# Kernel optimization log

Measured on AMD Instinct MI355X. Metric: run time of the kernel, lower is better.

The kernel has to match this reference:

```python
import jax, jax.numpy as jnp
import numpy as np
from jax import lax

SQRT_HALF = np.float32(np.sqrt(0.5))


def glu_block(x, pad_mask, w, b):
    # x: [B,T,D], pad_mask: [B,T] True=padded, w: [2D,D,3], b: [2D]
    x = jnp.where(pad_mask[..., None], 0.0, x)
    xc = jnp.transpose(x, (0, 2, 1))  # [B,D,T]
    y = lax.conv_general_dilated(xc, w, (1,), 'SAME',
                                 dimension_numbers=('NCH', 'OIH', 'NCH'))
    y = y + b[None, :, None]
    y = jnp.transpose(y, (0, 2, 1))  # [B,T,2D]
    a, g = jnp.split(y, 2, axis=-1)
    out = a * jax.nn.sigmoid(g)
    return (out + x) * SQRT_HALF


def setup_inputs() -> dict:
    key = jax.random.key(0)
    ks = jax.random.split(key, 12)
    B, T_MEL, T_PH, D, V, MEL_D = 32, 2000, 512, 256, 100, 80
    mels = jax.random.normal(ks[0], (B, T_MEL, MEL_D), dtype=jnp.float32)
    phonemes = jax.random.randint(ks[1], (B, T_PH), 0, V)
    mel_lens = jax.random.randint(ks[2], (B,), 1, T_MEL)
    phoneme_lens = jax.random.randint(ks[3], (B,), 1, T_PH)
    embedding = 0.02 * jax.random.normal(ks[4], (V, D), dtype=jnp.float32)
    mel_conv_w = 0.02 * jax.random.normal(ks[5], (D, MEL_D, 3), dtype=jnp.float32)
    mel_conv_b = jnp.zeros((D,), dtype=jnp.float32)
    ph_w = 0.02 * jax.random.normal(ks[6], (4, 2 * D, D, 3), dtype=jnp.float32)
    ph_b = jnp.zeros((4, 2 * D), dtype=jnp.float32)
    mel_w = 0.02 * jax.random.normal(ks[7], (4, 2 * D, D, 3), dtype=jnp.float32)
    mel_b = jnp.zeros((4, 2 * D), dtype=jnp.float32)
    return {"mels": mels, "phonemes": phonemes, "mel_lens": mel_lens,
            "phoneme_lens": phoneme_lens, "embedding": embedding,
            "mel_conv_w": mel_conv_w, "mel_conv_b": mel_conv_b,
            "ph_w": ph_w, "ph_b": ph_b, "mel_w": mel_w, "mel_b": mel_b}


def reference(mels, phonemes, mel_lens, phoneme_lens, embedding,
              mel_conv_w, mel_conv_b, ph_w, ph_b, mel_w, mel_b):
    B, T_mel, _ = mels.shape
    # --- mel encoder ---
    mel_mask = jnp.arange(T_mel)[None, :] >= mel_lens[:, None]  # [B,T_mel]
    mc = lax.conv_general_dilated(jnp.transpose(mels, (0, 2, 1)), mel_conv_w,
                                  (1,), 'SAME',
                                  dimension_numbers=('NCH', 'OIH', 'NCH'))
    mel_enc = jnp.transpose(mc + mel_conv_b[None, :, None], (0, 2, 1))
    for i in range(4):
        mel_enc = glu_block(mel_enc, mel_mask, mel_w[i], mel_b[i])
    # --- phoneme encoder (prepend blank index 0) ---
    ph = jnp.pad(phonemes, ((0, 0), (1, 0)), constant_values=0)  # [B,T_ph+1]
    T_ph1 = ph.shape[1]
    ph_mask = jnp.arange(T_ph1)[None, :] > phoneme_lens[:, None]  # [B,T_ph+1]
    ph_enc = embedding[ph]  # [B,T_ph+1,D]
    for i in range(4):
        ph_enc = glu_block(ph_enc, ph_mask, ph_w[i], ph_b[i])
    # --- negative squared pairwise L2 distances, masked over padded phonemes ---
    mel_sq = jnp.sum(mel_enc * mel_enc, axis=-1)  # [B,T_mel]
    ph_sq = jnp.sum(ph_enc * ph_enc, axis=-1)     # [B,T_ph+1]
    dots = jnp.einsum('btd,bsd->bts', mel_enc, ph_enc)  # [B,T_mel,T_ph+1]
    distances = 2.0 * dots - mel_sq[:, :, None] - ph_sq[:, None, :]
    distances = jnp.where(ph_mask[:, None, :], -1e9, distances)
    attn = jax.nn.softmax(distances, axis=2)
    context = jnp.einsum('bts,bsd->btd', attn, ph_enc)
    return jnp.concatenate([mel_enc, context], axis=2)  # [B,T_mel,2D]
```

## Files before the change

### kernel.cpp

```cpp
#include <hip/hip_runtime.h>

typedef _Float16 f16;
typedef __attribute__((ext_vector_type(8))) _Float16 half8;
typedef __attribute__((ext_vector_type(4))) _Float16 half4;
typedef __attribute__((ext_vector_type(4))) float f32x4;

__device__ inline f32x4 mfma16(half8 a, half8 b, f32x4 c) {
  return __builtin_amdgcn_mfma_f32_16x16x32_f16(a, b, c, 0, 0, 0);
}

__global__ void prep_wtglu_kernel(const float* __restrict__ mel_w,
                                  const float* __restrict__ ph_w,
                                  f16* __restrict__ wt) {
  int bid = blockIdx.x;
  int p = bid % 12, lby = bid / 12;
  int by = lby & 3, l = lby >> 2;
  int cb = p / 3, tap = p - cb * 3;
  const float* src = (l < 4) ? (mel_w + (size_t)l * 512 * 256 * 3)
                             : (ph_w + (size_t)(l - 4) * 512 * 256 * 3);
  f16* dst = wt + (size_t)bid * 8192;
  int tid = threadIdx.x;
#pragma unroll
  for (int k = 0; k < 4; ++k) {
    int s = tid + k * 256;
    int lane = s & 63, rest = s >> 6;
    int kc = rest & 1, nt = (rest >> 1) & 3, wc = rest >> 3;
    int rg = by * 128 + wc * 64 + nt * 16 + (lane & 15);
    int n32 = rg >> 5, j = rg & 31;
    int ch = (j < 16) ? (n32 * 16 + j) : (256 + n32 * 16 + (j - 16));
    int i0 = cb * 64 + kc * 32 + (lane >> 4) * 8;
#pragma unroll
    for (int e = 0; e < 8; ++e)
      dst[(size_t)s * 8 + e] = (f16)src[((size_t)ch * 256 + i0 + e) * 3 + tap];
  }
}

__global__ void prep_wt0_kernel(const float* __restrict__ w, f16* __restrict__ wt0) {
  int idx = blockIdx.x * 256 + threadIdx.x;
  const int total = 256 * 288;
  if (idx >= total) return;
  int o = idx / 288, k = idx % 288;
  int tap = k / 96, i = k % 96;
  wt0[idx] = (i < 80) ? (f16)w[((size_t)o * 80 + i) * 3 + tap] : (f16)0.f;
}

__global__ void embed_kernel(const int* __restrict__ phon, const float* __restrict__ emb,
                             f16* __restrict__ out) {
  int s = blockIdx.x, b = blockIdx.y;
  int lane = threadIdx.x;
  int tok = (s == 0) ? 0 : phon[b * 512 + (s - 1)];
  float4 f = *(const float4*)(emb + (size_t)tok * 256 + lane * 4);
  half4 h = {(f16)f.x, (f16)f.y, (f16)f.z, (f16)f.w};
  *(half4*)(out + ((size_t)b * 513 + s) * 256 + lane * 4) = h;
}

__global__ __launch_bounds__(256) void conv0_kernel(
    const float* __restrict__ mels, const f16* __restrict__ wt0,
    const float* __restrict__ bias, f16* __restrict__ out) {
  __shared__ f16 xs[66 * 104];
  __shared__ f16 ws[64 * 104];
  const int tid = threadIdx.x;
  const int b = blockIdx.z;
  const int t0 = blockIdx.x * 64;
  const int by = blockIdx.y;

  for (int idx = tid; idx < 66 * 24; idx += 256) {
    int r = idx / 24, v = idx % 24;
    int t = t0 - 1 + r;
    half4 h = {0.f, 0.f, 0.f, 0.f};
    if (t >= 0 && t < 2000 && v < 20) {
      float4 f = *(const float4*)(mels + ((size_t)b * 2000 + t) * 80 + v * 4);
      h[0] = (f16)f.x; h[1] = (f16)f.y; h[2] = (f16)f.z; h[3] = (f16)f.w;
    }
    *(half4*)(xs + r * 104 + v * 4) = h;
  }
  const int lane = tid & 63, wv = tid >> 6;
  const int wr = wv >> 1, wc = wv & 1;
  const int l15 = lane & 15, q = lane >> 4;
  f32x4 acc[2][2] = {};
  const f16* wrow = wt0 + (size_t)(by * 64) * 288;
  for (int tap = 0; tap < 3; ++tap) {
    __syncthreads();
    for (int idx = tid; idx < 64 * 12; idx += 256) {
      int r = idx / 12, v = idx % 12;
      *(half8*)(ws + r * 104 + v * 8) =
          *(const half8*)(wrow + (size_t)r * 288 + tap * 96 + v * 8);
    }
    __syncthreads();
#pragma unroll
    for (int s2 = 0; s2 < 3; ++s2) {
      int ch = s2 * 32 + q * 8;
      half8 a0 = *(const half8*)(xs + (32 * wr + l15 + tap) * 104 + ch);
      half8 a1 = *(const half8*)(xs + (32 * wr + 16 + l15 + tap) * 104 + ch);
      half8 b0 = *(const half8*)(ws + (32 * wc + l15) * 104 + ch);
      half8 b1 = *(const half8*)(ws + (32 * wc + 16 + l15) * 104 + ch);
      acc[0][0] = mfma16(a0, b0, acc[0][0]);
      acc[0][1] = mfma16(a0, b1, acc[0][1]);
      acc[1][0] = mfma16(a1, b0, acc[1][0]);
      acc[1][1] = mfma16(a1, b1, acc[1][1]);
    }
  }
#pragma unroll
  for (int rf = 0; rf < 2; ++rf)
#pragma unroll
    for (int cf = 0; cf < 2; ++cf) {
      int c = by * 64 + 32 * wc + 16 * cf + l15;
      float bb = bias[c];
#pragma unroll
      for (int r = 0; r < 4; ++r) {
        int t = t0 + 32 * wr + 16 * rf + 4 * q + r;
        if (t < 2000)
          out[((size_t)b * 2000 + t) * 256 + c] = (f16)(acc[rf][cf][r] + bb);
      }
    }
}

__device__ __forceinline__ void glu_body(
    f16* xs,
    const f16* __restrict__ x, const f16* __restrict__ wt,
    const float* __restrict__ bias, f16* __restrict__ out,
    const int* __restrict__ lens, int lenAdd, int T, int TT, int writeConst,
    int bx, int by, int b) {
  const int tid = threadIdx.x;
  const int tt = (bx + b) % TT;
  const int t0 = tt * 128;
  int thr = lens[b] + lenAdd;
  if (thr > T) thr = T;
  const size_t xbase = (size_t)b * T * 256;
  const int lane = tid & 63, wv = tid >> 6;
  const int wr = wv >> 1, wc = wv & 1;
  const int l15 = lane & 15, q = lane >> 4;

  if (t0 > thr) {
    if (writeConst) {
#pragma unroll
      for (int p = 0; p < 2; ++p) {
        int n32 = by * 4 + wc * 2 + p;
        int c = n32 * 16 + l15;
        float ba = bias[c], bg = bias[256 + c];
        f16 o = (f16)((ba * (1.0f / (1.0f + __expf(-bg)))) * 0.70710678118f);
#pragma unroll
        for (int mt = 0; mt < 4; ++mt)
#pragma unroll
          for (int rr = 0; rr < 4; ++rr) {
            int t = t0 + wr * 64 + mt * 16 + q * 4 + rr;
            if (t < T) out[xbase + (size_t)t * 256 + c] = o;
          }
      }
    }
    return;
  }

  f32x4 acc[4][4] = {};
  const f16* wby = wt + (size_t)by * 12 * 8192 + (size_t)wc * 4096 + (size_t)lane * 8;

  half8 xr[5];
  half8 wb[4][2], wn[4][2];
  auto loadX = [&](int cb) {
#pragma unroll
    for (int it = 0; it < 5; ++it) {
      int idx = tid + it * 256;
      half8 val = {};
      if (idx < 1040) {
        int lr = idx >> 3, v = idx & 7;
        int trow = t0 - 1 + lr;
        if (trow >= 0 && trow < thr)
          val = *(const half8*)(x + xbase + (size_t)trow * 256 + cb * 64 + v * 8);
      }
      xr[it] = val;
    }
  };
  auto storeX = [&]() {
#pragma unroll
    for (int it = 0; it < 5; ++it) {
      int idx = tid + it * 256;
      if (idx < 1040) {
        int lr = idx >> 3, v = idx & 7;
        *(half8*)(xs + lr * 72 + v * 8) = xr[it];
      }
    }
  };
  auto loadWreg = [&](half8 W[4][2], int p) {
    const f16* wp = wby + (size_t)p * 8192;
#pragma unroll
    for (int nt = 0; nt < 4; ++nt)
#pragma unroll
      for (int kc = 0; kc < 2; ++kc)
        W[nt][kc] = *(const half8*)(wp + (nt * 2 + kc) * 512);
  };

  loadX(0);
  loadWreg(wb, 0);

#pragma unroll
  for (int cb = 0; cb < 4; ++cb) {
    __syncthreads();
    storeX();
    __syncthreads();
    if (cb < 3) loadX(cb + 1);
#pragma unroll
    for (int tap = 0; tap < 3; ++tap) {
      const int p = cb * 3 + tap;
      if (p < 11) loadWreg(wn, p + 1);

      half8 af[4][2];
#pragma unroll
      for (int mt = 0; mt < 4; ++mt)
#pragma unroll
        for (int kc = 0; kc < 2; ++kc)
          af[mt][kc] = *(const half8*)(xs + (wr * 64 + mt * 16 + l15 + tap) * 72 + kc * 32 + q * 8);
      __builtin_amdgcn_s_setprio(1);
#pragma unroll
      for (int nt = 0; nt < 4; ++nt)
#pragma unroll
        for (int mt = 0; mt < 4; ++mt) {
          acc[mt][nt] = mfma16(af[mt][0], wb[nt][0], acc[mt][nt]);
          acc[mt][nt] = mfma16(af[mt][1], wb[nt][1], acc[mt][nt]);
        }
      __builtin_amdgcn_s_setprio(0);
#pragma unroll
      for (int nt = 0; nt < 4; ++nt) {
        wb[nt][0] = wn[nt][0];
        wb[nt][1] = wn[nt][1];
      }
    }
  }

#pragma unroll
  for (int p = 0; p < 2; ++p) {
    int n32 = by * 4 + wc * 2 + p;
    int c = n32 * 16 + l15;
    float ba = bias[c], bg = bias[256 + c];
#pragma unroll
    for (int mt = 0; mt < 4; ++mt) {
#pragma unroll
      for (int rr = 0; rr < 4; ++rr) {
        int t = t0 + wr * 64 + mt * 16 + q * 4 + rr;
        if (t < T && (writeConst || t < thr)) {
          float a = acc[mt][2 * p][rr] + ba;
          float g = acc[mt][2 * p + 1][rr] + bg;
          float xm = (t < thr) ? (float)x[xbase + (size_t)t * 256 + c] : 0.f;
          float o = (a * (1.0f / (1.0f + __expf(-g))) + xm) * 0.70710678118f;
          out[xbase + (size_t)t * 256 + c] = (f16)o;
        }
      }
    }
  }
}

__global__ __launch_bounds__(256) void glu_fused_kernel(
    const f16* __restrict__ xm, const f16* __restrict__ wtm,
    const float* __restrict__ bm, f16* __restrict__ om,
    const int* __restrict__ mlens,
    const f16* __restrict__ xp, const f16* __restrict__ wtp,
    const float* __restrict__ bp, f16* __restrict__ op,
    const int* __restrict__ plens, int writeConst) {
  __shared__ f16 xs[132 * 72];
  const int lin = blockIdx.x;
  if (lin < 2048) {
    int b = lin >> 6, y = (lin >> 4) & 3, x = lin & 15;
    glu_body(xs, xm, wtm, bm, om, mlens, 0, 2000, 16, writeConst, x, y, b);
  } else {
    int l2 = lin - 2048;
    int b = l2 / 20, r = l2 % 20, y = r / 5, x = r % 5;
    glu_body(xs, xp, wtp, bp, op, plens, 1, 513, 5, writeConst, x, y, b);
  }
}

__global__ __launch_bounds__(256) void transpose_kernel(const f16* __restrict__ ph,
                                                        f16* __restrict__ phT) {
  __shared__ f16 tile[64 * 72];
  const int tid = threadIdx.x;
  const int b = blockIdx.z, s0 = blockIdx.x * 64, d0 = blockIdx.y * 64;
#pragma unroll
  for (int it = 0; it < 2; ++it) {
    int idx = tid + it * 256;
    int r = idx >> 3, v = idx & 7;
    int s = s0 + r;
    half8 val = {};
    if (s < 513) val = *(const half8*)(ph + ((size_t)b * 513 + s) * 256 + d0 + v * 8);
    *(half8*)(tile + r * 72 + v * 8) = val;
  }
  __syncthreads();
#pragma unroll
  for (int it = 0; it < 2; ++it) {
    int idx = tid + it * 256;
    int r = idx >> 3, v = idx & 7;
    half8 val;
#pragma unroll
    for (int j2 = 0; j2 < 8; ++j2) val[j2] = tile[(v * 8 + j2) * 72 + r];
    *(half8*)(phT + ((size_t)b * 256 + d0 + r) * 576 + s0 + v * 8) = val;
  }
}

__global__ void sqnorm_kernel(const f16* __restrict__ x, float* __restrict__ sq, int nrows) {
  int row = blockIdx.x * 4 + (threadIdx.x >> 6);
  int lane = threadIdx.x & 63;
  if (row >= nrows) return;
  const f16* p = x + (size_t)row * 256;
  float v = 0.f;
  for (int i = lane; i < 256; i += 64) { float f = (float)p[i]; v += f * f; }
  for (int off = 32; off > 0; off >>= 1) v += __shfl_down(v, off);
  if (lane == 0) sq[row] = v;
}

__global__ __launch_bounds__(256) void flash_kernel(
    const f16* __restrict__ mel, const f16* __restrict__ ph,
    const f16* __restrict__ phT, const float* __restrict__ phsq,
    const int* __restrict__ plens, float* __restrict__ out) {
  __shared__ f16 vt[256 * 72];
  __shared__ f16 ps[4][16 * 72];
  __shared__ float phs[576];
  const int tid = threadIdx.x;
  const int lin = blockIdx.x;
  const int b = ((lin >> 8) << 3) | (lin & 7);
  const int t0 = ((lin >> 3) & 31) * 64;
  const int lane = tid & 63, wv = tid >> 6;
  const int l15 = lane & 15, q = lane >> 4;
  const int plen = plens[b];
  const int nkt = (plen + 64) >> 6;

  for (int idx = tid; idx < 576; idx += 256)
    phs[idx] = (idx < 513) ? phsq[b * 513 + idx] : 0.f;

  const int tq = t0 + 16 * wv + l15;
  half8 qf[8];
  {
    const f16* qrow = mel + ((size_t)b * 2000 + ((tq < 2000) ? tq : 0)) * 256;
#pragma unroll
    for (int c = 0; c < 8; ++c) qf[c] = *(const half8*)(qrow + c * 32 + q * 8);
    if (tq >= 2000) {
      half8 z = {};
#pragma unroll
      for (int c = 0; c < 8; ++c) qf[c] = z;
    }
  }
  if (tq < 2000) {
    float* orow = out + ((size_t)b * 2000 + tq) * 512;
#pragma unroll
    for (int c = 0; c < 8; ++c) {
      half8 h = qf[c];
      float4 f0 = {(float)h[0], (float)h[1], (float)h[2], (float)h[3]};
      float4 f1 = {(float)h[4], (float)h[5], (float)h[6], (float)h[7]};
      *(float4*)(orow + c * 32 + q * 8) = f0;
      *(float4*)(orow + c * 32 + q * 8 + 4) = f1;
    }
  }

  half8 vreg[8];
  const int d_st = tid >> 3, v_st = tid & 7;
  auto loadV = [&](int kt) {
#pragma unroll
    for (int it = 0; it < 8; ++it) {
      int d = d_st + 32 * it;
      vreg[it] = *(const half8*)(phT + ((size_t)b * 256 + d) * 576 + kt * 64 + v_st * 8);
    }
  };
  loadV(0);

  float mr[4], lr[4];
#pragma unroll
  for (int r = 0; r < 4; ++r) { mr[r] = -3.0e38f; lr[r] = 0.f; }
  f32x4 acc[16] = {};
  f16* pw = ps[wv];

#pragma unroll 1
  for (int kt = 0; kt < nkt; ++kt) {
    const int s0 = kt * 64;
    __syncthreads();
#pragma unroll
    for (int it = 0; it < 8; ++it)
      *(half8*)(vt + (d_st + 32 * it) * 72 + v_st * 8) = vreg[it];
    __syncthreads();
    if (kt + 1 < nkt) loadV(kt + 1);

    const f16* krow[4];
#pragma unroll
    for (int cf = 0; cf < 4; ++cf)
      krow[cf] = ph + ((size_t)b * 513 + (s0 + cf * 16 + l15)) * 256 + q * 8;
    f32x4 sc[4] = {};
    __builtin_amdgcn_s_setprio(1);
#pragma unroll
    for (int c = 0; c < 8; ++c) {
#pragma unroll
      for (int cf = 0; cf < 4; ++cf) {
        half8 bf = *(const half8*)(krow[cf] + c * 32);
        sc[cf] = mfma16(qf[c], bf, sc[cf]);
      }
    }
    __builtin_amdgcn_s_setprio(0);
    float p[4][4];
    float rmax[4] = {-3.0e38f, -3.0e38f, -3.0e38f, -3.0e38f};
#pragma unroll
    for (int cf = 0; cf < 4; ++cf) {
      int sloc = cf * 16 + l15;
      int s = s0 + sloc;
      bool msk = (s > plen) || (s >= 513);
      float p2 = phs[s0 + sloc];
#pragma unroll
      for (int r = 0; r < 4; ++r) {
        float v = 2.0f * sc[cf][r] - p2;
        if (msk) v = -1.0e9f;
        p[cf][r] = v;
        rmax[r] = fmaxf(rmax[r], v);
      }
    }
#pragma unroll
    for (int r = 0; r < 4; ++r)
#pragma unroll
      for (int off = 1; off < 16; off <<= 1)
        rmax[r] = fmaxf(rmax[r], __shfl_xor(rmax[r], off));
    float alpha[4];
#pragma unroll
    for (int r = 0; r < 4; ++r) {
      float mn = fmaxf(mr[r], rmax[r]);
      alpha[r] = __expf(mr[r] - mn);
      mr[r] = mn;
      float rs = 0.f;
#pragma unroll
      for (int cf = 0; cf < 4; ++cf) {
        float e = __expf(p[cf][r] - mn);
        p[cf][r] = e;
        rs += e;
      }
#pragma unroll
      for (int off = 1; off < 16; off <<= 1) rs += __shfl_xor(rs, off);
      lr[r] = lr[r] * alpha[r] + rs;
    }
#pragma unroll
    for (int dt = 0; dt < 16; ++dt)
#pragma unroll
      for (int r = 0; r < 4; ++r) acc[dt][r] *= alpha[r];
#pragma unroll
    for (int cf = 0; cf < 4; ++cf)
#pragma unroll
      for (int r = 0; r < 4; ++r)
        pw[(q * 4 + r) * 72 + cf * 16 + l15] = (f16)p[cf][r];
#pragma unroll
    for (int kc = 0; kc < 2; ++kc) {
      half8 pa = *(const half8*)(pw + l15 * 72 + kc * 32 + q * 8);
      __builtin_amdgcn_s_setprio(1);
#pragma unroll
      for (int dt = 0; dt < 16; ++dt) {
        half8 vb = *(const half8*)(vt + (dt * 16 + l15) * 72 + kc * 32 + q * 8);
        acc[dt] = mfma16(pa, vb, acc[dt]);
      }
      __builtin_amdgcn_s_setprio(0);
    }
  }
  float inv[4];
#pragma unroll
  for (int r = 0; r < 4; ++r) inv[r] = 1.0f / lr[r];
#pragma unroll
  for (int dt = 0; dt < 16; ++dt)
#pragma unroll
    for (int r = 0; r < 4; ++r) {
      int t = t0 + 16 * wv + q * 4 + r;
      if (t < 2000) {
        int d = dt * 16 + l15;
        out[((size_t)b * 2000 + t) * 512 + 256 + d] = acc[dt][r] * inv[r];
      }
    }
}

extern "C" void kernel_launch(void* const* d_in, const int* in_sizes, int n_in,
                              void* d_out, int out_size, void* d_ws, size_t ws_size,
                              hipStream_t stream) {
  (void)in_sizes; (void)n_in; (void)out_size; (void)ws_size;
  const float* mels       = (const float*)d_in[0];
  const int*   phonemes   = (const int*)d_in[1];
  const int*   mel_lens   = (const int*)d_in[2];
  const int*   ph_lens    = (const int*)d_in[3];
  const float* embedding  = (const float*)d_in[4];
  const float* mel_conv_w = (const float*)d_in[5];
  const float* mel_conv_b = (const float*)d_in[6];
  const float* ph_w       = (const float*)d_in[7];
  const float* ph_b       = (const float*)d_in[8];
  const float* mel_w      = (const float*)d_in[9];
  const float* mel_b      = (const float*)d_in[10];
  float* out = (float*)d_out;

  char* wsp = (char*)d_ws;
  size_t off = 0;
  auto alloc = [&](size_t bytes) -> void* {
    void* p = wsp + off;
    off = (off + bytes + 255) & ~(size_t)255;
    return p;
  };
  f16* wtg    = (f16*)alloc(8ull * 4 * 12 * 8192 * 2);
  f16* wt0    = (f16*)alloc(256ull * 288 * 2);
  float* phsq = (float*)alloc(16416ull * 4);
  f16* p0     = (f16*)alloc(32ull * 513 * 256 * 2);
  f16* p1     = (f16*)alloc(32ull * 513 * 256 * 2);
  f16* m0     = (f16*)alloc(32ull * 2000 * 256 * 2);
  f16* m1     = (f16*)alloc(32ull * 2000 * 256 * 2);
  f16* phT = m1;

  prep_wtglu_kernel<<<384, 256, 0, stream>>>(mel_w, ph_w, wtg);
  prep_wt0_kernel<<<288, 256, 0, stream>>>(mel_conv_w, wt0);
  embed_kernel<<<dim3(513, 32), 64, 0, stream>>>(phonemes, embedding, p0);
  conv0_kernel<<<dim3(32, 4, 32), 256, 0, stream>>>(mels, wt0, mel_conv_b, m0);

  const size_t WL = 4ull * 12 * 8192;
  glu_fused_kernel<<<2688, 256, 0, stream>>>(
      m0, wtg + 0 * WL, mel_b + 0 * 512, m1, mel_lens,
      p0, wtg + 4 * WL, ph_b + 0 * 512, p1, ph_lens, 0);
  glu_fused_kernel<<<2688, 256, 0, stream>>>(
      m1, wtg + 1 * WL, mel_b + 1 * 512, m0, mel_lens,
      p1, wtg + 5 * WL, ph_b + 1 * 512, p0, ph_lens, 0);
  glu_fused_kernel<<<2688, 256, 0, stream>>>(
      m0, wtg + 2 * WL, mel_b + 2 * 512, m1, mel_lens,
      p0, wtg + 6 * WL, ph_b + 2 * 512, p1, ph_lens, 0);
  glu_fused_kernel<<<2688, 256, 0, stream>>>(
      m1, wtg + 3 * WL, mel_b + 3 * 512, m0, mel_lens,
      p1, wtg + 7 * WL, ph_b + 3 * 512, p0, ph_lens, 1);

  transpose_kernel<<<dim3(9, 4, 32), 256, 0, stream>>>(p0, phT);
  sqnorm_kernel<<<4104, 256, 0, stream>>>(p0, phsq, 16416);
  flash_kernel<<<dim3(32 * 32), 256, 0, stream>>>(m0, p0, phT, phsq, ph_lens, out);
}
```

Baseline: 614.5 us.

## Pre-swizzle V into MFMA fragment layout and read it directly from global

The transpose kernel now writes the phoneme encoding in the exact per-lane MFMA B-fragment order, so the flash kernel can load V fragments straight from global/L2 with coalesced half8 loads. This removes the V staging through LDS, the two block-wide barriers per key tile, and the register prefetch. In exchange each wave reads V independently from global memory (four times the traffic into L2 per block), and nothing is prefetched ahead, so load latency may be exposed in the PV matmul.

Result: slower. 638.1 us (+3.8%).

```diff
diff --git a/kernel.cpp b/kernel.cpp
--- a/kernel.cpp
+++ b/kernel.cpp
@@ -268,10 +268,11 @@
 }
 
 __global__ __launch_bounds__(256) void transpose_kernel(const f16* __restrict__ ph,
-                                                        f16* __restrict__ phT) {
+                                                        f16* __restrict__ vf) {
   __shared__ f16 tile[64 * 72];
   const int tid = threadIdx.x;
-  const int b = blockIdx.z, s0 = blockIdx.x * 64, d0 = blockIdx.y * 64;
+  const int b = blockIdx.z, kt = blockIdx.x, dg = blockIdx.y;
+  const int s0 = kt * 64, d0 = dg * 64;
 #pragma unroll
   for (int it = 0; it < 2; ++it) {
     int idx = tid + it * 256;
@@ -284,12 +285,17 @@
   __syncthreads();
 #pragma unroll
   for (int it = 0; it < 2; ++it) {
-    int idx = tid + it * 256;
-    int r = idx >> 3, v = idx & 7;
+    int sIdx = tid + it * 256;
+    int lane = sIdx & 63, rest = sIdx >> 6;
+    int kc = rest & 1, dtl = rest >> 1;
+    int q = lane >> 4, l15 = lane & 15;
     half8 val;
 #pragma unroll
-    for (int j2 = 0; j2 < 8; ++j2) val[j2] = tile[(v * 8 + j2) * 72 + r];
-    *(half8*)(phT + ((size_t)b * 256 + d0 + r) * 576 + s0 + v * 8) = val;
+    for (int e = 0; e < 8; ++e)
+      val[e] = tile[(kc * 32 + q * 8 + e) * 72 + dtl * 16 + l15];
+    int dt = dg * 4 + dtl;
+    *(half8*)(vf + (size_t)b * 147456 +
+              ((((size_t)kt * 16 + dt) * 2 + kc) * 64 + lane) * 8) = val;
   }
 }
 
@@ -306,9 +312,8 @@
 
 __global__ __launch_bounds__(256) void flash_kernel(
     const f16* __restrict__ mel, const f16* __restrict__ ph,
-    const f16* __restrict__ phT, const float* __restrict__ phsq,
+    const f16* __restrict__ vf, const float* __restrict__ phsq,
     const int* __restrict__ plens, float* __restrict__ out) {
-  __shared__ f16 vt[256 * 72];
   __shared__ f16 ps[4][16 * 72];
   __shared__ float phs[576];
   const int tid = threadIdx.x;
@@ -346,34 +351,18 @@
       *(float4*)(orow + c * 32 + q * 8 + 4) = f1;
     }
   }
-
-  half8 vreg[8];
-  const int d_st = tid >> 3, v_st = tid & 7;
-  auto loadV = [&](int kt) {
-#pragma unroll
-    for (int it = 0; it < 8; ++it) {
-      int d = d_st + 32 * it;
-      vreg[it] = *(const half8*)(phT + ((size_t)b * 256 + d) * 576 + kt * 64 + v_st * 8);
-    }
-  };
-  loadV(0);
+  __syncthreads();
 
   float mr[4], lr[4];
 #pragma unroll
   for (int r = 0; r < 4; ++r) { mr[r] = -3.0e38f; lr[r] = 0.f; }
   f32x4 acc[16] = {};
   f16* pw = ps[wv];
+  const f16* vfb = vf + (size_t)b * 147456 + (size_t)lane * 8;
 
 #pragma unroll 1
   for (int kt = 0; kt < nkt; ++kt) {
     const int s0 = kt * 64;
-    __syncthreads();
-#pragma unroll
-    for (int it = 0; it < 8; ++it)
-      *(half8*)(vt + (d_st + 32 * it) * 72 + v_st * 8) = vreg[it];
-    __syncthreads();
-    if (kt + 1 < nkt) loadV(kt + 1);
-
     const f16* krow[4];
 #pragma unroll
     for (int cf = 0; cf < 4; ++cf)
@@ -436,13 +425,14 @@
 #pragma unroll
       for (int r = 0; r < 4; ++r)
         pw[(q * 4 + r) * 72 + cf * 16 + l15] = (f16)p[cf][r];
+    const f16* vkt = vfb + (size_t)kt * 16384;
 #pragma unroll
     for (int kc = 0; kc < 2; ++kc) {
       half8 pa = *(const half8*)(pw + l15 * 72 + kc * 32 + q * 8);
       __builtin_amdgcn_s_setprio(1);
 #pragma unroll
       for (int dt = 0; dt < 16; ++dt) {
-        half8 vb = *(const half8*)(vt + (dt * 16 + l15) * 72 + kc * 32 + q * 8);
+        half8 vb = *(const half8*)(vkt + (dt * 2 + kc) * 512);
         acc[dt] = mfma16(pa, vb, acc[dt]);
       }
       __builtin_amdgcn_s_setprio(0);
@@ -494,7 +484,7 @@
   f16* p1     = (f16*)alloc(32ull * 513 * 256 * 2);
   f16* m0     = (f16*)alloc(32ull * 2000 * 256 * 2);
   f16* m1     = (f16*)alloc(32ull * 2000 * 256 * 2);
-  f16* phT = m1;
+  f16* vf  = m1;
 
   prep_wtglu_kernel<<<384, 256, 0, stream>>>(mel_w, ph_w, wtg);
   prep_wt0_kernel<<<288, 256, 0, stream>>>(mel_conv_w, wt0);
@@ -515,7 +505,7 @@
       m1, wtg + 3 * WL, mel_b + 3 * 512, m0, mel_lens,
       p1, wtg + 7 * WL, ph_b + 3 * 512, p0, ph_lens, 1);
 
-  transpose_kernel<<<dim3(9, 4, 32), 256, 0, stream>>>(p0, phT);
+  transpose_kernel<<<dim3(9, 4, 32), 256, 0, stream>>>(p0, vf);
   sqnorm_kernel<<<4104, 256, 0, stream>>>(p0, phsq, 16416);
-  flash_kernel<<<dim3(32 * 32), 256, 0, stream>>>(m0, p0, phT, phsq, ph_lens, out);
-}
+  flash_kernel<<<dim3(32 * 32), 256, 0, stream>>>(m0, p0, vf, phsq, ph_lens, out);
+}
```
